# Kernel optimization log

Hardware: AMD Instinct MI355X
Metric: run time of the kernel (lower is better)

## Reference

```python
import jax, jax.numpy as jnp
import numpy as np

B, NODE, DEG, K = 16, 32, 64, 8
IN_F, OUT_F, SUP = 128, 3, 10
FEATS = [96, 256, 256, 256, 128, 128]
SIZES = [1, 2, 4, 8, 16, 32]


def setup_inputs() -> dict:
    key = jax.random.key(0)
    ks = jax.random.split(key, 20)
    d = {}
    for i in range(6):
        d[f"t{i}"] = jax.random.normal(ks[i], (B, SIZES[i], FEATS[i]), jnp.float32)
    for i in range(6):
        d[f"Wr{i}"] = jax.random.normal(ks[6 + i], (FEATS[i], OUT_F), jnp.float32) * 0.1
    d["W_branch"] = jax.random.normal(ks[12], (NODE, IN_F, DEG * IN_F), jnp.float32) * 0.02
    d["Wl1"] = jax.random.normal(ks[13], (IN_F, IN_F * SUP), jnp.float32) * 0.05
    d["Wl2"] = jax.random.normal(ks[14], (IN_F * SUP, OUT_F), jnp.float32) * 0.02
    d["bias"] = jax.random.uniform(ks[15], (1, DEG, OUT_F), jnp.float32, -0.5, 0.5)
    d["c1w"] = jax.random.normal(ks[16], (64, 6), jnp.float32) * 0.2
    d["c1b"] = jnp.zeros((64,), jnp.float32)
    d["c2w"] = jax.random.normal(ks[17], (3, 64), jnp.float32) * 0.1
    d["c2b"] = jnp.zeros((3,), jnp.float32)
    return d


def _leaky(x):
    return jnp.where(x >= 0, x, 0.2 * x)  # LeakyReLU(0.2)


def reference(t0, t1, t2, t3, t4, t5, Wr0, Wr1, Wr2, Wr3, Wr4, Wr5,
              W_branch, Wl1, Wl2, bias, c1w, c1b, c2w, c2b):
    trees = [t0, t1, t2, t3, t4, t5]
    Wrs = [Wr0, Wr1, Wr2, Wr3, Wr4, Wr5]

    # --- root aggregation: per-ancestor linear + contiguous tiling to `node` rows ---
    root = jnp.zeros((B, NODE, OUT_F), jnp.float32)
    for t, W in zip(trees, Wrs):
        rn = t.shape[1]
        root = root + jnp.repeat(t @ W, NODE // rn, axis=1)  # (B, NODE, 3)

    # --- branch upsample: per-node weight matrix, then 2-layer loop MLP ---
    branch = _leaky(jnp.einsum('bni,nio->bno', t5, W_branch))  # (B, NODE, DEG*IN_F)
    branch = branch.reshape(B, NODE * DEG, IN_F)
    branch = (branch @ Wl1) @ Wl2  # (B, N, 3)
    branch = jnp.repeat(root, DEG, axis=1) + branch  # (B, N, 3), N = NODE*DEG

    # --- EdgeConv: knn on 3-d points, gather, 1x1 convs, max over neighbors ---
    x = branch  # (B, N, 3) point coordinates
    xx = jnp.sum(x * x, axis=-1)  # (B, N)
    inner = jnp.einsum('bnc,bmc->bnm', x, x)  # (B, N, N)
    pd = 2.0 * inner - xx[:, :, None] - xx[:, None, :]  # -squared distance
    _, idx = jax.lax.top_k(pd, K)  # (B, N, K) nearest-neighbor indices

    feat = x[jnp.arange(B)[:, None, None], idx]  # (B, N, K, 3) gather
    center = jnp.broadcast_to(x[:, :, None, :], feat.shape)
    g = jnp.concatenate([feat - center, center], axis=-1)  # (B, N, K, 6)

    h = jnp.einsum('bnkc,oc->bnko', g, c1w) + c1b  # conv1 1x1: 6 -> 64
    h = jnp.einsum('bnko,po->bnkp', h, c2w) + c2b  # conv2 1x1: 64 -> 3
    h = jnp.max(h, axis=2)  # max over K neighbors -> (B, N, 3)

    out = _leaky(h + jnp.tile(bias, (1, NODE, 1)))  # bias (1, DEG, 3) tiled to (1, N, 3)
    return out
```

## Files before the change

kernel.cpp:

```cpp
#include <hip/hip_runtime.h>
#include <float.h>

#define B_    16
#define NODE_ 32
#define DEG_  64
#define KNN_  8
#define ROWS_ 2048

#define OFF_X     0
#define OFF_Y     131072
#define OFF_ROOT  (OFF_Y + 4194304)
#define OFF_WL12  (OFF_ROOT + 2048)
#define OFF_EFF   (OFF_WL12 + 512)

__device__ __forceinline__ float med3f(float a, float b, float c) {
    return __builtin_amdgcn_fmed3f(a, b, c);
}
__device__ __forceinline__ float leaky(float v) { return v >= 0.f ? v : 0.2f * v; }

__global__ __launch_bounds__(128) void kA(
    const float* __restrict__ t0, const float* __restrict__ t1, const float* __restrict__ t2,
    const float* __restrict__ t3, const float* __restrict__ t4, const float* __restrict__ t5,
    const float* __restrict__ Wr0, const float* __restrict__ Wr1, const float* __restrict__ Wr2,
    const float* __restrict__ Wr3, const float* __restrict__ Wr4, const float* __restrict__ Wr5,
    const float* __restrict__ Wl1, const float* __restrict__ Wl2,
    const float* __restrict__ c1w, const float* __restrict__ c1b,
    const float* __restrict__ c2w, const float* __restrict__ c2b,
    float* __restrict__ ws)
{
    const int blk = blockIdx.x, tid = threadIdx.x;
    if (blk == 0) {
        const float* wp = Wl1 + tid * 1280;
        float a0 = 0.f, a1 = 0.f, a2 = 0.f;
        for (int s = 0; s < 1280; ++s) {
            float w = wp[s];
            a0 = fmaf(w, Wl2[s * 3 + 0], a0);
            a1 = fmaf(w, Wl2[s * 3 + 1], a1);
            a2 = fmaf(w, Wl2[s * 3 + 2], a2);
        }
        float* o = ws + OFF_WL12 + tid * 4;
        o[0] = a0; o[1] = a1; o[2] = a2; o[3] = 0.f;
    } else if (blk <= 12) {
        int idx = (blk - 1) * 128 + tid;
        int c = idx % 3, n = (idx / 3) & 31, b = idx / 96;
        float acc = 0.f;
#define TREE(T, W, RN, F) { \
        const float* tp = T + (b * RN + ((n * RN) >> 5)) * F; \
        for (int k = 0; k < F; ++k) acc = fmaf(tp[k], W[k * 3 + c], acc); }
        TREE(t0, Wr0, 1, 96)
        TREE(t1, Wr1, 2, 256)
        TREE(t2, Wr2, 4, 256)
        TREE(t3, Wr3, 8, 256)
        TREE(t4, Wr4, 16, 128)
        TREE(t5, Wr5, 32, 128)
#undef TREE
        ws[OFF_ROOT + (b * 32 + n) * 4 + c] = acc;
    } else {
        if (tid < 18) {
            int p = tid / 6, c = tid % 6;
            float a = 0.f;
            for (int o = 0; o < 64; ++o) a = fmaf(c2w[p * 64 + o], c1w[o * 6 + c], a);
            ws[OFF_EFF + tid] = a;
        } else if (tid < 21) {
            int p = tid - 18;
            float a = c2b[p];
            for (int o = 0; o < 64; ++o) a = fmaf(c2w[p * 64 + o], c1b[o], a);
            ws[OFF_EFF + 24 + p] = a;
        }
    }
}

__global__ __launch_bounds__(256) void kB1(const float* __restrict__ t5,
                                           const float* __restrict__ Wb,
                                           float* __restrict__ ws)
{
    const int n = blockIdx.x >> 5, jt = blockIdx.x & 31, tid = threadIdx.x;
    __shared__ float ts[128 * 16];
    for (int q = tid; q < 2048; q += 256) {
        int b = q >> 7, k = q & 127;
        ts[k * 16 + b] = t5[b * 4096 + n * 128 + k];
    }
    __syncthreads();
    const int j  = jt * 256 + ((tid & 63) << 2);
    const int bq = tid >> 6;
    const float* wp = Wb + n * 1048576 + j;
    float4 acc0 = {0,0,0,0}, acc1 = {0,0,0,0}, acc2 = {0,0,0,0}, acc3 = {0,0,0,0};
#pragma unroll 4
    for (int k = 0; k < 128; ++k) {
        float4 wv = *(const float4*)(wp + k * 8192);
        float4 tb = *(const float4*)(ts + k * 16 + bq * 4);
        acc0.x = fmaf(tb.x, wv.x, acc0.x); acc0.y = fmaf(tb.x, wv.y, acc0.y);
        acc0.z = fmaf(tb.x, wv.z, acc0.z); acc0.w = fmaf(tb.x, wv.w, acc0.w);
        acc1.x = fmaf(tb.y, wv.x, acc1.x); acc1.y = fmaf(tb.y, wv.y, acc1.y);
        acc1.z = fmaf(tb.y, wv.z, acc1.z); acc1.w = fmaf(tb.y, wv.w, acc1.w);
        acc2.x = fmaf(tb.z, wv.x, acc2.x); acc2.y = fmaf(tb.z, wv.y, acc2.y);
        acc2.z = fmaf(tb.z, wv.z, acc2.z); acc2.w = fmaf(tb.z, wv.w, acc2.w);
        acc3.x = fmaf(tb.w, wv.x, acc3.x); acc3.y = fmaf(tb.w, wv.y, acc3.y);
        acc3.z = fmaf(tb.w, wv.z, acc3.z); acc3.w = fmaf(tb.w, wv.w, acc3.w);
    }
    float* yb = ws + OFF_Y + n * 8192 + j;
#define STY(A, BI) { float4 y = make_float4(leaky(A.x), leaky(A.y), leaky(A.z), leaky(A.w)); \
                     *(float4*)(yb + (size_t)(4 * bq + BI) * 262144) = y; }
    STY(acc0, 0) STY(acc1, 1) STY(acc2, 2) STY(acc3, 3)
#undef STY
}

__global__ __launch_bounds__(256) void kB2(float* __restrict__ ws)
{
    __shared__ float wl[512];
    const int tid = threadIdx.x;
    for (int q = tid; q < 512; q += 256) wl[q] = ws[OFF_WL12 + q];
    __syncthreads();
    const int gid = blockIdx.x * 256 + tid;
    const int b = gid >> 11, r = gid & 2047, n = r >> 6;
    const float* rt = ws + OFF_ROOT + ((b * 32 + n) << 2);
    float x0 = rt[0], x1 = rt[1], x2 = rt[2];
    const float4* yp = (const float4*)(ws + OFF_Y + (size_t)(b * 32 + n) * 8192 + ((r & 63) << 7));
#pragma unroll 8
    for (int i4 = 0; i4 < 32; ++i4) {
        float4 y = yp[i4];
        const float4* wr = ((const float4*)wl) + (i4 << 2);
        float4 w0 = wr[0], w1 = wr[1], w2 = wr[2], w3 = wr[3];
        x0 = fmaf(y.x, w0.x, x0); x0 = fmaf(y.y, w1.x, x0); x0 = fmaf(y.z, w2.x, x0); x0 = fmaf(y.w, w3.x, x0);
        x1 = fmaf(y.x, w0.y, x1); x1 = fmaf(y.y, w1.y, x1); x1 = fmaf(y.z, w2.y, x1); x1 = fmaf(y.w, w3.y, x1);
        x2 = fmaf(y.x, w0.z, x2); x2 = fmaf(y.y, w1.z, x2); x2 = fmaf(y.z, w2.z, x2); x2 = fmaf(y.w, w3.z, x2);
    }
    float xx = fmaf(x0, x0, fmaf(x1, x1, x2 * x2));
    ((float4*)(ws + OFF_X))[gid] = make_float4(x0, x1, x2, xx);
}

#define CAP_ 16
#define CSWAPD(a, b) { float _hi = fmaxf(a, b), _lo = fminf(a, b); a = _hi; b = _lo; }
#define INS8(P, s0,s1,s2,s3,s4,s5,s6,s7) \
    s7 = med3f(P, s7, s6); s6 = med3f(P, s6, s5); \
    s5 = med3f(P, s5, s4); s4 = med3f(P, s4, s3); \
    s3 = med3f(P, s3, s2); s2 = med3f(P, s2, s1); \
    s1 = med3f(P, s1, s0); s0 = fmaxf(s0, P);
#define MERGE8(W, s0,s1,s2,s3,s4,s5,s6,s7) { \
    float o0 = __shfl_xor(s0, W), o1 = __shfl_xor(s1, W), o2 = __shfl_xor(s2, W), o3 = __shfl_xor(s3, W); \
    float o4 = __shfl_xor(s4, W), o5 = __shfl_xor(s5, W), o6 = __shfl_xor(s6, W), o7 = __shfl_xor(s7, W); \
    float n0 = fmaxf(s0, o7), n1 = fmaxf(s1, o6), n2 = fmaxf(s2, o5), n3 = fmaxf(s3, o4); \
    float n4 = fmaxf(s4, o3), n5 = fmaxf(s5, o2), n6 = fmaxf(s6, o1), n7 = fmaxf(s7, o0); \
    CSWAPD(n0, n4) CSWAPD(n1, n5) CSWAPD(n2, n6) CSWAPD(n3, n7) \
    CSWAPD(n0, n2) CSWAPD(n1, n3) CSWAPD(n4, n6) CSWAPD(n5, n7) \
    CSWAPD(n0, n1) CSWAPD(n2, n3) CSWAPD(n4, n5) CSWAPD(n6, n7) \
    s0 = n0; s1 = n1; s2 = n2; s3 = n3; s4 = n4; s5 = n5; s6 = n6; s7 = n7; }
#define PD(XR, XM) fmaf(2.f, fmaf(XR.x, XM.x, fmaf(XR.y, XM.y, XR.z * XM.z)), -(XR.w + XM.w))

__global__ __launch_bounds__(256) void kC(const float* __restrict__ ws,
                                          const float* __restrict__ bias,
                                          float* __restrict__ out)
{
    const int bb = blockIdx.x >> 6, rtile = blockIdx.x & 63, tid = threadIdx.x;
    __shared__ float4 xs[2048];
    __shared__ float eff[32];
    __shared__ int cnt[32];
    __shared__ int lists[32][CAP_];
    __shared__ int sel[32][KNN_];

    const float4* xg = (const float4*)(ws + OFF_X) + bb * 2048;
    for (int q = tid; q < 2048; q += 256) xs[q] = xg[q];
    if (tid < 32) { eff[tid] = ws[OFF_EFF + tid]; cnt[tid] = 0; }
    __syncthreads();

    const int g  = tid >> 5;
    const int mp = tid & 31;
    const int r0 = rtile * 32 + g * 4;
    const float4 xa = xs[r0], xb = xs[r0 + 1], xc = xs[r0 + 2], xd = xs[r0 + 3];

    float A0=-FLT_MAX,A1=-FLT_MAX,A2=-FLT_MAX,A3=-FLT_MAX,A4=-FLT_MAX,A5=-FLT_MAX,A6=-FLT_MAX,A7=-FLT_MAX;
    float B0=-FLT_MAX,B1=-FLT_MAX,B2=-FLT_MAX,B3=-FLT_MAX,B4=-FLT_MAX,B5=-FLT_MAX,B6=-FLT_MAX,B7=-FLT_MAX;
    float C0=-FLT_MAX,C1=-FLT_MAX,C2=-FLT_MAX,C3=-FLT_MAX,C4=-FLT_MAX,C5=-FLT_MAX,C6=-FLT_MAX,C7=-FLT_MAX;
    float D0=-FLT_MAX,D1=-FLT_MAX,D2=-FLT_MAX,D3=-FLT_MAX,D4=-FLT_MAX,D5=-FLT_MAX,D6=-FLT_MAX,D7=-FLT_MAX;

#pragma unroll 4
    for (int mm = 0; mm < 64; ++mm) {
        float4 xm = xs[(mm << 5) | mp];
        float pa = PD(xa, xm); INS8(pa, A0,A1,A2,A3,A4,A5,A6,A7)
        float pb = PD(xb, xm); INS8(pb, B0,B1,B2,B3,B4,B5,B6,B7)
        float pc = PD(xc, xm); INS8(pc, C0,C1,C2,C3,C4,C5,C6,C7)
        float pdv = PD(xd, xm); INS8(pdv, D0,D1,D2,D3,D4,D5,D6,D7)
    }
#pragma unroll
    for (int w = 1; w < 32; w <<= 1) {
        MERGE8(w, A0,A1,A2,A3,A4,A5,A6,A7)
        MERGE8(w, B0,B1,B2,B3,B4,B5,B6,B7)
        MERGE8(w, C0,C1,C2,C3,C4,C5,C6,C7)
        MERGE8(w, D0,D1,D2,D3,D4,D5,D6,D7)
    }
    const float Ta = A7, Tb = B7, Tc = C7, Td = D7;

#pragma unroll 4
    for (int mm = 0; mm < 64; ++mm) {
        int m = (mm << 5) | mp;
        float4 xm = xs[m];
        float pa = PD(xa, xm);
        float pb = PD(xb, xm);
        float pc = PD(xc, xm);
        float pdv = PD(xd, xm);
        if (pa >= Ta) { int s = atomicAdd(&cnt[g*4+0], 1); if (s < CAP_) lists[g*4+0][s] = m | ((pa > Ta) ? 0x10000 : 0); }
        if (pb >= Tb) { int s = atomicAdd(&cnt[g*4+1], 1); if (s < CAP_) lists[g*4+1][s] = m | ((pb > Tb) ? 0x10000 : 0); }
        if (pc >= Tc) { int s = atomicAdd(&cnt[g*4+2], 1); if (s < CAP_) lists[g*4+2][s] = m | ((pc > Tc) ? 0x10000 : 0); }
        if (pdv >= Td){ int s = atomicAdd(&cnt[g*4+3], 1); if (s < CAP_) lists[g*4+3][s] = m | ((pdv > Td) ? 0x10000 : 0); }
    }
    __syncthreads();

    const int lr = tid >> 3;
    const int part = tid & 7;
    const int r = rtile * 32 + lr;
    if (part == 0) {
        int c = cnt[lr]; if (c > CAP_) c = CAP_;
        int ng = 0;
        for (int q = 0; q < c; ++q) {
            int v = lists[lr][q];
            if (v & 0x10000) sel[lr][ng++] = v & 0xFFFF;
        }
        int prev = -1;
        while (ng < KNN_) {
            int best = 0x7FFFFFFF;
            for (int q = 0; q < c; ++q) {
                int v = lists[lr][q];
                if (!(v & 0x10000)) {
                    int m = v & 0xFFFF;
                    if (m > prev && m < best) best = m;
                }
            }
            if (best == 0x7FFFFFFF) best = r;
            sel[lr][ng++] = best; prev = best;
        }
    }
    __syncthreads();

    const float4 xr = xs[r];
    const int ms = sel[lr][part];
    const float4 fm = xs[ms];
    const float g0 = fm.x - xr.x, g1 = fm.y - xr.y, g2 = fm.z - xr.z;
    float h0 = eff[24], h1 = eff[25], h2 = eff[26];
    h0 = fmaf(g0, eff[0], h0);  h0 = fmaf(g1, eff[1], h0);  h0 = fmaf(g2, eff[2], h0);
    h0 = fmaf(xr.x, eff[3], h0); h0 = fmaf(xr.y, eff[4], h0); h0 = fmaf(xr.z, eff[5], h0);
    h1 = fmaf(g0, eff[6], h1);  h1 = fmaf(g1, eff[7], h1);  h1 = fmaf(g2, eff[8], h1);
    h1 = fmaf(xr.x, eff[9], h1); h1 = fmaf(xr.y, eff[10], h1); h1 = fmaf(xr.z, eff[11], h1);
    h2 = fmaf(g0, eff[12], h2); h2 = fmaf(g1, eff[13], h2); h2 = fmaf(g2, eff[14], h2);
    h2 = fmaf(xr.x, eff[15], h2); h2 = fmaf(xr.y, eff[16], h2); h2 = fmaf(xr.z, eff[17], h2);
#pragma unroll
    for (int w = 1; w < 8; w <<= 1) {
        h0 = fmaxf(h0, __shfl_xor(h0, w));
        h1 = fmaxf(h1, __shfl_xor(h1, w));
        h2 = fmaxf(h2, __shfl_xor(h2, w));
    }
    if (part == 0) {
        const float* bp = bias + (r & 63) * 3;
        float* op = out + (size_t)(bb * 2048 + r) * 3;
        op[0] = leaky(h0 + bp[0]);
        op[1] = leaky(h1 + bp[1]);
        op[2] = leaky(h2 + bp[2]);
    }
}

extern "C" void kernel_launch(void* const* d_in, const int* in_sizes, int n_in,
                              void* d_out, int out_size, void* d_ws, size_t ws_size,
                              hipStream_t stream)
{
    const float* t0 = (const float*)d_in[0];
    const float* t1 = (const float*)d_in[1];
    const float* t2 = (const float*)d_in[2];
    const float* t3 = (const float*)d_in[3];
    const float* t4 = (const float*)d_in[4];
    const float* t5 = (const float*)d_in[5];
    const float* Wr0 = (const float*)d_in[6];
    const float* Wr1 = (const float*)d_in[7];
    const float* Wr2 = (const float*)d_in[8];
    const float* Wr3 = (const float*)d_in[9];
    const float* Wr4 = (const float*)d_in[10];
    const float* Wr5 = (const float*)d_in[11];
    const float* Wb  = (const float*)d_in[12];
    const float* Wl1 = (const float*)d_in[13];
    const float* Wl2 = (const float*)d_in[14];
    const float* bias = (const float*)d_in[15];
    const float* c1w = (const float*)d_in[16];
    const float* c1b = (const float*)d_in[17];
    const float* c2w = (const float*)d_in[18];
    const float* c2b = (const float*)d_in[19];
    float* ws = (float*)d_ws;
    float* out = (float*)d_out;

    hipLaunchKernelGGL(kA, dim3(14), dim3(128), 0, stream,
                       t0, t1, t2, t3, t4, t5, Wr0, Wr1, Wr2, Wr3, Wr4, Wr5,
                       Wl1, Wl2, c1w, c1b, c2w, c2b, ws);
    hipLaunchKernelGGL(kB1, dim3(1024), dim3(256), 0, stream, t5, Wb, ws);
    hipLaunchKernelGGL(kB2, dim3(128), dim3(256), 0, stream, ws);
    hipLaunchKernelGGL(kC, dim3(1024), dim3(256), 0, stream, ws, bias, out);
}
```

Measured before the change: 354.0 us.

## Fuse branch GEMM with loop-MLP projection to drop the intermediate buffer

Merges the per-node branch GEMM (kB1) and the 128-to-3 projection (kB2) into one kernel. Each wave now owns one degree slot and reduces the leaky outputs against the folded Wl1·Wl2 weights through cross-lane shuffles, so the 16 MB intermediate Y is never written to or read back from global memory. The kernel also reorganises the work per thread (2 output columns by 16 batches instead of 4 columns by 4 batches). It parallelises the Wl1·Wl2 precompute across 8 blocks with wave reductions where a single block did it before. In exchange it adds a large number of shuffle reductions per wave and raises register pressure from 32 accumulators.

Measured after the change: 326.1 us. 1.09x faster.

```diff
diff --git a/kernel.cpp b/kernel.cpp
--- a/kernel.cpp
+++ b/kernel.cpp
@@ -8,8 +8,7 @@
 #define ROWS_ 2048
 
 #define OFF_X     0
-#define OFF_Y     131072
-#define OFF_ROOT  (OFF_Y + 4194304)
+#define OFF_ROOT  131072
 #define OFF_WL12  (OFF_ROOT + 2048)
 #define OFF_EFF   (OFF_WL12 + 512)
 
@@ -18,7 +17,7 @@
 }
 __device__ __forceinline__ float leaky(float v) { return v >= 0.f ? v : 0.2f * v; }
 
-__global__ __launch_bounds__(128) void kA(
+__global__ __launch_bounds__(256) void kA(
     const float* __restrict__ t0, const float* __restrict__ t1, const float* __restrict__ t2,
     const float* __restrict__ t3, const float* __restrict__ t4, const float* __restrict__ t5,
     const float* __restrict__ Wr0, const float* __restrict__ Wr1, const float* __restrict__ Wr2,
@@ -29,19 +28,33 @@
     float* __restrict__ ws)
 {
     const int blk = blockIdx.x, tid = threadIdx.x;
-    if (blk == 0) {
-        const float* wp = Wl1 + tid * 1280;
-        float a0 = 0.f, a1 = 0.f, a2 = 0.f;
-        for (int s = 0; s < 1280; ++s) {
-            float w = wp[s];
-            a0 = fmaf(w, Wl2[s * 3 + 0], a0);
-            a1 = fmaf(w, Wl2[s * 3 + 1], a1);
-            a2 = fmaf(w, Wl2[s * 3 + 2], a2);
-        }
-        float* o = ws + OFF_WL12 + tid * 4;
-        o[0] = a0; o[1] = a1; o[2] = a2; o[3] = 0.f;
-    } else if (blk <= 12) {
-        int idx = (blk - 1) * 128 + tid;
+    if (blk < 8) {
+        const int lane = tid & 63;
+        const int ibase = blk * 16 + (tid >> 6) * 4;
+#pragma unroll
+        for (int ii = 0; ii < 4; ++ii) {
+            const float* wp = Wl1 + (size_t)(ibase + ii) * 1280;
+            float a0 = 0.f, a1 = 0.f, a2 = 0.f;
+            for (int s5 = 0; s5 < 20; ++s5) {
+                int s = s5 * 64 + lane;
+                float w = wp[s];
+                a0 = fmaf(w, Wl2[s * 3 + 0], a0);
+                a1 = fmaf(w, Wl2[s * 3 + 1], a1);
+                a2 = fmaf(w, Wl2[s * 3 + 2], a2);
+            }
+#pragma unroll
+            for (int d = 1; d < 64; d <<= 1) {
+                a0 += __shfl_xor(a0, d);
+                a1 += __shfl_xor(a1, d);
+                a2 += __shfl_xor(a2, d);
+            }
+            if (lane == 0) {
+                float* o = ws + OFF_WL12 + (ibase + ii) * 4;
+                o[0] = a0; o[1] = a1; o[2] = a2; o[3] = 0.f;
+            }
+        }
+    } else if (blk < 14) {
+        int idx = (blk - 8) * 256 + tid;
         int c = idx % 3, n = (idx / 3) & 31, b = idx / 96;
         float acc = 0.f;
 #define TREE(T, W, RN, F) { \
@@ -70,63 +83,72 @@
     }
 }
 
-__global__ __launch_bounds__(256) void kB1(const float* __restrict__ t5,
+__global__ __launch_bounds__(256) void kBX(const float* __restrict__ t5,
                                            const float* __restrict__ Wb,
                                            float* __restrict__ ws)
 {
-    const int n = blockIdx.x >> 5, jt = blockIdx.x & 31, tid = threadIdx.x;
-    __shared__ float ts[128 * 16];
+    const int n = blockIdx.x >> 4, jt = blockIdx.x & 15, tid = threadIdx.x;
+    __shared__ float ts[2048];
     for (int q = tid; q < 2048; q += 256) {
         int b = q >> 7, k = q & 127;
         ts[k * 16 + b] = t5[b * 4096 + n * 128 + k];
     }
     __syncthreads();
-    const int j  = jt * 256 + ((tid & 63) << 2);
-    const int bq = tid >> 6;
-    const float* wp = Wb + n * 1048576 + j;
-    float4 acc0 = {0,0,0,0}, acc1 = {0,0,0,0}, acc2 = {0,0,0,0}, acc3 = {0,0,0,0};
+    const int w = tid >> 6, lane = tid & 63;
+    const int d = jt * 4 + w;
+    const int i0 = lane * 2;
+    const float* wp = Wb + (size_t)n * 1048576 + d * 128 + i0;
+
+    float acc[16][2];
+#pragma unroll
+    for (int b = 0; b < 16; ++b) { acc[b][0] = 0.f; acc[b][1] = 0.f; }
+
 #pragma unroll 4
     for (int k = 0; k < 128; ++k) {
-        float4 wv = *(const float4*)(wp + k * 8192);
-        float4 tb = *(const float4*)(ts + k * 16 + bq * 4);
-        acc0.x = fmaf(tb.x, wv.x, acc0.x); acc0.y = fmaf(tb.x, wv.y, acc0.y);
-        acc0.z = fmaf(tb.x, wv.z, acc0.z); acc0.w = fmaf(tb.x, wv.w, acc0.w);
-        acc1.x = fmaf(tb.y, wv.x, acc1.x); acc1.y = fmaf(tb.y, wv.y, acc1.y);
-        acc1.z = fmaf(tb.y, wv.z, acc1.z); acc1.w = fmaf(tb.y, wv.w, acc1.w);
-        acc2.x = fmaf(tb.z, wv.x, acc2.x); acc2.y = fmaf(tb.z, wv.y, acc2.y);
-        acc2.z = fmaf(tb.z, wv.z, acc2.z); acc2.w = fmaf(tb.z, wv.w, acc2.w);
-        acc3.x = fmaf(tb.w, wv.x, acc3.x); acc3.y = fmaf(tb.w, wv.y, acc3.y);
-        acc3.z = fmaf(tb.w, wv.z, acc3.z); acc3.w = fmaf(tb.w, wv.w, acc3.w);
-    }
-    float* yb = ws + OFF_Y + n * 8192 + j;
-#define STY(A, BI) { float4 y = make_float4(leaky(A.x), leaky(A.y), leaky(A.z), leaky(A.w)); \
-                     *(float4*)(yb + (size_t)(4 * bq + BI) * 262144) = y; }
-    STY(acc0, 0) STY(acc1, 1) STY(acc2, 2) STY(acc3, 3)
-#undef STY
-}
-
-__global__ __launch_bounds__(256) void kB2(float* __restrict__ ws)
-{
-    __shared__ float wl[512];
-    const int tid = threadIdx.x;
-    for (int q = tid; q < 512; q += 256) wl[q] = ws[OFF_WL12 + q];
-    __syncthreads();
-    const int gid = blockIdx.x * 256 + tid;
-    const int b = gid >> 11, r = gid & 2047, n = r >> 6;
-    const float* rt = ws + OFF_ROOT + ((b * 32 + n) << 2);
-    float x0 = rt[0], x1 = rt[1], x2 = rt[2];
-    const float4* yp = (const float4*)(ws + OFF_Y + (size_t)(b * 32 + n) * 8192 + ((r & 63) << 7));
-#pragma unroll 8
-    for (int i4 = 0; i4 < 32; ++i4) {
-        float4 y = yp[i4];
-        const float4* wr = ((const float4*)wl) + (i4 << 2);
-        float4 w0 = wr[0], w1 = wr[1], w2 = wr[2], w3 = wr[3];
-        x0 = fmaf(y.x, w0.x, x0); x0 = fmaf(y.y, w1.x, x0); x0 = fmaf(y.z, w2.x, x0); x0 = fmaf(y.w, w3.x, x0);
-        x1 = fmaf(y.x, w0.y, x1); x1 = fmaf(y.y, w1.y, x1); x1 = fmaf(y.z, w2.y, x1); x1 = fmaf(y.w, w3.y, x1);
-        x2 = fmaf(y.x, w0.z, x2); x2 = fmaf(y.y, w1.z, x2); x2 = fmaf(y.z, w2.z, x2); x2 = fmaf(y.w, w3.z, x2);
-    }
-    float xx = fmaf(x0, x0, fmaf(x1, x1, x2 * x2));
-    ((float4*)(ws + OFF_X))[gid] = make_float4(x0, x1, x2, xx);
+        float2 wv = *(const float2*)(wp + (size_t)k * 8192);
+        const float4* tk = (const float4*)(ts + (k << 4));
+        float4 t0v = tk[0], t1v = tk[1], t2v = tk[2], t3v = tk[3];
+#define FM(BI, TV) acc[BI][0] = fmaf(TV, wv.x, acc[BI][0]); acc[BI][1] = fmaf(TV, wv.y, acc[BI][1]);
+        FM(0, t0v.x) FM(1, t0v.y) FM(2, t0v.z) FM(3, t0v.w)
+        FM(4, t1v.x) FM(5, t1v.y) FM(6, t1v.z) FM(7, t1v.w)
+        FM(8, t2v.x) FM(9, t2v.y) FM(10, t2v.z) FM(11, t2v.w)
+        FM(12, t3v.x) FM(13, t3v.y) FM(14, t3v.z) FM(15, t3v.w)
+#undef FM
+    }
+
+    const float4 wl0 = *(const float4*)(ws + OFF_WL12 + i0 * 4);
+    const float4 wl1 = *(const float4*)(ws + OFF_WL12 + (i0 + 1) * 4);
+    float P[16][3];
+#pragma unroll
+    for (int b = 0; b < 16; ++b) {
+        float y0 = leaky(acc[b][0]), y1 = leaky(acc[b][1]);
+        P[b][0] = fmaf(y1, wl1.x, y0 * wl0.x);
+        P[b][1] = fmaf(y1, wl1.y, y0 * wl0.y);
+        P[b][2] = fmaf(y1, wl1.z, y0 * wl0.z);
+    }
+#pragma unroll
+    for (int b = 0; b < 16; ++b) {
+#pragma unroll
+        for (int dd = 1; dd < 64; dd <<= 1) {
+            P[b][0] += __shfl_xor(P[b][0], dd);
+            P[b][1] += __shfl_xor(P[b][1], dd);
+            P[b][2] += __shfl_xor(P[b][2], dd);
+        }
+    }
+    float q0 = P[0][0], q1 = P[0][1], q2 = P[0][2];
+#pragma unroll
+    for (int b = 1; b < 16; ++b) {
+        bool m = (lane == b);
+        q0 = m ? P[b][0] : q0;
+        q1 = m ? P[b][1] : q1;
+        q2 = m ? P[b][2] : q2;
+    }
+    if (lane < 16) {
+        float4 rt = ((const float4*)(ws + OFF_ROOT))[lane * 32 + n];
+        float x0 = rt.x + q0, x1 = rt.y + q1, x2 = rt.z + q2;
+        float xx = fmaf(x0, x0, fmaf(x1, x1, x2 * x2));
+        ((float4*)(ws + OFF_X))[lane * 2048 + n * 64 + d] = make_float4(x0, x1, x2, xx);
+    }
 }
 
 #define CAP_ 16
@@ -284,10 +306,9 @@
     float* ws = (float*)d_ws;
     float* out = (float*)d_out;
 
-    hipLaunchKernelGGL(kA, dim3(14), dim3(128), 0, stream,
+    hipLaunchKernelGGL(kA, dim3(15), dim3(256), 0, stream,
                        t0, t1, t2, t3, t4, t5, Wr0, Wr1, Wr2, Wr3, Wr4, Wr5,
                        Wl1, Wl2, c1w, c1b, c2w, c2b, ws);
-    hipLaunchKernelGGL(kB1, dim3(1024), dim3(256), 0, stream, t5, Wb, ws);
-    hipLaunchKernelGGL(kB2, dim3(128), dim3(256), 0, stream, ws);
+    hipLaunchKernelGGL(kBX, dim3(512), dim3(256), 0, stream, t5, Wb, ws);
     hipLaunchKernelGGL(kC, dim3(1024), dim3(256), 0, stream, ws, bias, out);
 }
```
